# Optimization experiments

Measured on AMD Instinct MI355X. Metric: run time of the kernel, lower is better.

The kernel has to match this reference:

```python
import jax, jax.numpy as jnp
import numpy as np

N = 50000      # nodes
E = 1_600_000  # edges (avg degree 32)
G = 2000       # graphs in batch
H = 2          # attention heads
C = 64         # out_channels
IN = 64        # in_channels
NEG_SLOPE = 0.2


def setup_inputs() -> dict:
    key = jax.random.key(0)
    ks = jax.random.split(key, 6)
    x = jax.random.normal(ks[0], (N, IN), dtype=jnp.float32)
    edge_index = jax.random.randint(ks[1], (2, E), 0, N, dtype=jnp.int32)
    batch = jnp.sort(jax.random.randint(ks[2], (N,), 0, G, dtype=jnp.int32))
    # GATConv params: lin weight [H*C, IN] (glorot-ish), att vectors, bias [C]
    W = jax.random.normal(ks[3], (H * C, IN), dtype=jnp.float32) * (1.0 / np.sqrt(IN))
    att_src = jax.random.normal(ks[4], (1, H, C), dtype=jnp.float32) * 0.1
    att_dst = jax.random.normal(ks[5], (1, H, C), dtype=jnp.float32) * 0.1
    bias = jnp.zeros((C,), dtype=jnp.float32)
    return {"x": x, "edge_index": edge_index, "batch": batch,
            "W": W, "att_src": att_src, "att_dst": att_dst, "bias": bias}


def reference(x, edge_index, batch, W, att_src, att_dst, bias):
    # --- GATConv (PyG semantics: add_self_loops=True, concat=False -> head mean + bias) ---
    loops = jnp.arange(N, dtype=edge_index.dtype)
    src = jnp.concatenate([edge_index[0], loops])  # [E+N]
    dst = jnp.concatenate([edge_index[1], loops])  # [E+N]

    xp = (x @ W.T).reshape(N, H, C)                 # projected node feats [N,H,C]
    a_src = jnp.sum(xp * att_src, axis=-1)          # [N,H]
    a_dst = jnp.sum(xp * att_dst, axis=-1)          # [N,H]

    e = jax.nn.leaky_relu(a_src[src] + a_dst[dst], NEG_SLOPE)  # [E+N,H]
    # segment softmax over incoming edges of each destination node
    m = jax.ops.segment_max(e, dst, num_segments=N)            # [N,H]
    e = jnp.exp(e - m[dst])
    s = jax.ops.segment_sum(e, dst, num_segments=N)            # [N,H]
    alpha = e / s[dst]                                         # [E+N,H]

    msg = xp[src] * alpha[:, :, None]                          # [E+N,H,C]
    out = jax.ops.segment_sum(msg, dst, num_segments=N)        # [N,H,C]
    h_nodes = out.mean(axis=1) + bias                          # [N,C]

    # --- global_mean_pool ---
    sums = jax.ops.segment_sum(h_nodes, batch, num_segments=G)                     # [G,C]
    cnt = jax.ops.segment_sum(jnp.ones((N, 1), h_nodes.dtype), batch, num_segments=G)
    h_graphs = sums / jnp.maximum(cnt, 1.0)                                        # [G,C]
    return (h_nodes, h_graphs)
```

## Files before the change

### kernel.cpp

```cpp
#include <hip/hip_runtime.h>
#include <hip/hip_bf16.h>

#define H 2
#define C 64
#define IN_CH 64
#define HC (H*C)
#define NEG_SLOPE 0.2f
#define NBUCK_MAX 1024
#define SBLK 512
#define BKT 64
#define CAP 3072

__global__ __launch_bounds__(128) void proj_kernel(
    const float* __restrict__ x, const float* __restrict__ W,
    const float* __restrict__ att_src, const float* __restrict__ att_dst,
    const int* __restrict__ batch, __hip_bfloat16* __restrict__ xp,
    float* __restrict__ asrc, float* __restrict__ adst, int* __restrict__ cnt,
    int* __restrict__ gbeg, int N, int nbuck, int G) {
    int t = threadIdx.x;
    if (blockIdx.x == 0)
        for (int i = t; i < nbuck; i += 128) cnt[i] = 0;
    {
        int i = blockIdx.x * 128 + t;
        if (i < N) {
            int bi = batch[i];
            if (i == 0) {
                for (int g = 0; g <= bi; g++) gbeg[g] = 0;
            } else {
                int bp = batch[i - 1];
                for (int g = bp + 1; g <= bi; g++) gbeg[g] = i;
            }
            if (i == N - 1)
                for (int g = bi + 1; g <= G; g++) gbeg[g] = N;
        }
    }
    float w[64];
    const float4* wr = reinterpret_cast<const float4*>(W + (size_t)t * IN_CH);
#pragma unroll
    for (int q = 0; q < 16; q++) {
        float4 v = wr[q];
        w[4 * q] = v.x; w[4 * q + 1] = v.y; w[4 * q + 2] = v.z; w[4 * q + 3] = v.w;
    }
    float a_s = att_src[t], a_d = att_dst[t];
    int lane = t & 63, head = t >> 6;
    for (int n = blockIdx.x; n < N; n += gridDim.x) {
        const float* xr = x + (size_t)n * IN_CH;
        float acc = 0.f;
#pragma unroll
        for (int k = 0; k < 64; k++) acc = fmaf(w[k], xr[k], acc);
        xp[(size_t)n * HC + t] = __float2bfloat16(acc);
        float as = acc * a_s, ad = acc * a_d;
#pragma unroll
        for (int d = 32; d > 0; d >>= 1) {
            as += __shfl_xor(as, d, 64);
            ad += __shfl_xor(ad, d, 64);
        }
        if (lane == 0) {
            asrc[(size_t)n * H + head] = as;
            adst[(size_t)n * H + head] = ad;
        }
    }
}

__global__ __launch_bounds__(256) void scatter_kernel(
    const int* __restrict__ edge, int* __restrict__ cnt,
    int* __restrict__ staged, int N, int E) {
    const int tid = threadIdx.x, bid = blockIdx.x;
    const int nbuck = (N + BKT - 1) / BKT;
    const int chunkE = (E + SBLK - 1) / SBLK;
    const int* srcE = edge;
    const int* dstE = edge + E;
    __shared__ int lh[NBUCK_MAX], bse[NBUCK_MAX], lcur[NBUCK_MAX];
    for (int i = tid; i < nbuck; i += 256) { lh[i] = 0; lcur[i] = 0; }
    __syncthreads();
    int beg = bid * chunkE, end = min(beg + chunkE, E);
    for (int i = beg + tid; i < end; i += 256)
        atomicAdd(&lh[dstE[i] >> 6], 1);
    __syncthreads();
    for (int i = tid; i < nbuck; i += 256)
        bse[i] = atomicAdd(&cnt[i], lh[i]);
    __syncthreads();
    for (int i = beg + tid; i < end; i += 256) {
        int s = srcE[i], d = dstE[i];
        int b = d >> 6;
        int l = atomicAdd(&lcur[b], 1);
        staged[(size_t)b * CAP + bse[b] + l] = s | ((d & 63) << 20);
    }
}

template<int NB>
__device__ __forceinline__ void gfma(const char* __restrict__ xb,
                                     const int* __restrict__ si,
                                     const float* __restrict__ swl,
                                     uint laneoff, float& accx, float& accy) {
    uint bu[NB];
#pragma unroll
    for (int j = 0; j < NB; j++) {
        uint boff = (uint)si[j] + laneoff;
        bu[j] = *reinterpret_cast<const uint*>(xb + boff);
    }
#pragma unroll
    for (int j = 0; j < NB; j++) {
        float w = swl[2 * j];
        accx = fmaf(w, __uint_as_float(bu[j] << 16), accx);
        accy = fmaf(w, __uint_as_float(bu[j] & 0xffff0000u), accy);
    }
}

__global__ __launch_bounds__(256, 4) void csragg_kernel(
    const __hip_bfloat16* __restrict__ xp, const float* __restrict__ asrc,
    const float* __restrict__ adst, const int* __restrict__ cnt,
    const int* __restrict__ staged_all, const float* __restrict__ bias,
    float* __restrict__ out, int N) {
    __shared__ int lcsr[CAP];
    __shared__ int loff[BKT + 1];
    __shared__ int lh[BKT], cur[BKT];
    __shared__ int sidx[4][32];
    __shared__ float swf[4][64];
    int b = blockIdx.x, tid = threadIdx.x;
    int lane = tid & 63, wid = tid >> 6;
    int size = cnt[b];
    const int* st = staged_all + (size_t)b * CAP;
    if (tid < BKT) lh[tid] = 0;
    __syncthreads();
    for (int i = tid; i < size; i += 256)
        atomicAdd(&lh[st[i] >> 20], 1);
    __syncthreads();
    if (wid == 0) {
        int v = lh[lane];
        int inc = v;
#pragma unroll
        for (int d = 1; d < 64; d <<= 1) {
            int u = __shfl_up(inc, d, 64);
            if (lane >= d) inc += u;
        }
        loff[lane] = inc - v;
        cur[lane] = inc - v;
        if (lane == 63) loff[BKT] = inc;
    }
    __syncthreads();
    for (int i = tid; i < size; i += 256) {
        int e = st[i];
        int pos = atomicAdd(&cur[e >> 20], 1);
        lcsr[pos] = (e & 0xFFFFF) << 8;
    }
    __syncthreads();
    const uint* xpw = reinterpret_cast<const uint*>(xp);
    const char* xb = reinterpret_cast<const char*>(xp);
    int cl = lane & 31, hsel = lane >> 5;
    uint laneoff = (uint)lane * 4u;
    int* si = sidx[wid];
    float* swl = swf[wid] + hsel;
    for (int k = 0; k < 16; k++) {
        int nd = wid * 16 + k;
        int n = b * BKT + nd;
        if (n >= N) break;
        int o0 = loff[nd];
        int deg = loff[nd + 1] - o0;
        float adh = adst[2 * n + hsel];
        float es = asrc[2 * n + hsel] + adh;
        es = (es > 0.f) ? es : NEG_SLOPE * es;
        float wself = __expf(es);
        float ssum = (cl == 0) ? wself : 0.f;
        uint u = xpw[(size_t)n * 64 + lane];
        float accx = wself * __uint_as_float(u << 16);
        float accy = wself * __uint_as_float(u & 0xffff0000u);
        for (int base = 0; base < deg; base += 32) {
            int i = base + cl;
            int boff = 0;
            float w = 0.f;
            if (i < deg) {
                boff = lcsr[o0 + i];
                float t = asrc[(boff >> 7) + hsel] + adh;
                t = (t > 0.f) ? t : NEG_SLOPE * t;
                w = __expf(t);
            }
            ssum += w;
            if (!hsel) si[cl] = boff;
            swl[2 * cl] = w;
            int nb = min(deg - base, 32);
            if (nb > 16) gfma<32>(xb, si, swl, laneoff, accx, accy);
            else         gfma<16>(xb, si, swl, laneoff, accx, accy);
        }
#pragma unroll
        for (int d = 16; d > 0; d >>= 1) ssum += __shfl_xor(ssum, d, 64);
        float inv = 1.f / ssum;
        accx *= inv;
        accy *= inv;
        float ox = 0.5f * (accx + __shfl_xor(accx, 32, 64));
        float oy = 0.5f * (accy + __shfl_xor(accy, 32, 64));
        if (lane < 32) {
            float vx = ox + bias[2 * cl];
            float vy = oy + bias[2 * cl + 1];
            *reinterpret_cast<float2*>(out + (size_t)n * C + 2 * cl) =
                make_float2(vx, vy);
        }
    }
}

__global__ __launch_bounds__(256) void pool_kernel(const float* __restrict__ hn,
                                                   const int* __restrict__ gbeg,
                                                   float* __restrict__ outG, int G) {
    int g = blockIdx.x;
    int c = threadIdx.x & 63, r = threadIdx.x >> 6;
    int beg = gbeg[g], end = gbeg[g + 1];
    float s = 0.f;
    for (int n = beg + r; n < end; n += 4) s += hn[(size_t)n * C + c];
    __shared__ float red[256];
    red[threadIdx.x] = s;
    __syncthreads();
    if (r == 0) {
        float tot = red[c] + red[64 + c] + red[128 + c] + red[192 + c];
        outG[(size_t)g * C + c] = tot / fmaxf((float)(end - beg), 1.f);
    }
}

extern "C" void kernel_launch(void* const* d_in, const int* in_sizes, int n_in,
                              void* d_out, int out_size, void* d_ws, size_t ws_size,
                              hipStream_t stream) {
    const float* x       = (const float*)d_in[0];
    const int*   edge    = (const int*)d_in[1];
    const int*   batch   = (const int*)d_in[2];
    const float* W       = (const float*)d_in[3];
    const float* att_src = (const float*)d_in[4];
    const float* att_dst = (const float*)d_in[5];
    const float* bias    = (const float*)d_in[6];

    int N = in_sizes[0] / IN_CH;
    int E = in_sizes[1] / 2;
    int G = out_size / C - N;
    int nbuck = (N + BKT - 1) / BKT;

    char* p = (char*)d_ws;
    auto alloc = [&](size_t bytes) {
        char* r = p;
        p += (bytes + 255) & ~(size_t)255;
        return r;
    };
    __hip_bfloat16* xp = (__hip_bfloat16*)alloc((size_t)N * HC * 2);
    float* asrc    = (float*)alloc((size_t)N * H * 4);
    float* adst    = (float*)alloc((size_t)N * H * 4);
    int*   cnt     = (int*)alloc((size_t)nbuck * 4);
    int*   staged  = (int*)alloc((size_t)nbuck * CAP * 4);
    int*   gbeg    = (int*)alloc((size_t)(G + 1) * 4);

    proj_kernel<<<2048, 128, 0, stream>>>(x, W, att_src, att_dst, batch, xp, asrc, adst,
                                          cnt, gbeg, N, nbuck, G);
    scatter_kernel<<<SBLK, 256, 0, stream>>>(edge, cnt, staged, N, E);
    csragg_kernel<<<nbuck, 256, 0, stream>>>(xp, asrc, adst, cnt, staged, bias,
                                             (float*)d_out, N);
    pool_kernel<<<G, 256, 0, stream>>>((const float*)d_out, gbeg,
                                       (float*)d_out + (size_t)N * C, G);
}
```

Baseline: 203.8 us.

## Merge projection and edge-scatter kernels into one launch with block specialization

The projection and edge bucket-scatter kernels are combined into one launch. The first 512 blocks do the scatter (now with 128 threads each instead of 256) and the remaining 2048 blocks do the projection, so the two independent stages can run at the same time. The bucket-count zeroing moves from the projection kernel to a hipMemsetAsync, because the scatter blocks now need cnt already cleared. This saves one kernel boundary and lets the stages overlap, but the scatter blocks have half the threads and the memset adds a small operation to the stream.

```diff
diff --git a/kernel.cpp b/kernel.cpp
--- a/kernel.cpp
+++ b/kernel.cpp
@@ -8,20 +8,44 @@
 #define NEG_SLOPE 0.2f
 #define NBUCK_MAX 1024
 #define SBLK 512
+#define PBLK 2048
 #define BKT 64
 #define CAP 3072
 
-__global__ __launch_bounds__(128) void proj_kernel(
+__global__ __launch_bounds__(128) void fused_kernel(
     const float* __restrict__ x, const float* __restrict__ W,
     const float* __restrict__ att_src, const float* __restrict__ att_dst,
-    const int* __restrict__ batch, __hip_bfloat16* __restrict__ xp,
-    float* __restrict__ asrc, float* __restrict__ adst, int* __restrict__ cnt,
-    int* __restrict__ gbeg, int N, int nbuck, int G) {
-    int t = threadIdx.x;
-    if (blockIdx.x == 0)
-        for (int i = t; i < nbuck; i += 128) cnt[i] = 0;
+    const int* __restrict__ batch, const int* __restrict__ edge,
+    __hip_bfloat16* __restrict__ xp, float* __restrict__ asrc,
+    float* __restrict__ adst, int* __restrict__ cnt, int* __restrict__ staged,
+    int* __restrict__ gbeg, int N, int E, int G, int nbuck) {
+    const int t = threadIdx.x;
+    if (blockIdx.x < SBLK) {
+        const int bid = blockIdx.x;
+        const int chunkE = (E + SBLK - 1) / SBLK;
+        const int* srcE = edge;
+        const int* dstE = edge + E;
+        __shared__ int lh[NBUCK_MAX], bse[NBUCK_MAX], lcur[NBUCK_MAX];
+        for (int i = t; i < nbuck; i += 128) { lh[i] = 0; lcur[i] = 0; }
+        __syncthreads();
+        int beg = bid * chunkE, end = min(beg + chunkE, E);
+        for (int i = beg + t; i < end; i += 128)
+            atomicAdd(&lh[dstE[i] >> 6], 1);
+        __syncthreads();
+        for (int i = t; i < nbuck; i += 128)
+            bse[i] = atomicAdd(&cnt[i], lh[i]);
+        __syncthreads();
+        for (int i = beg + t; i < end; i += 128) {
+            int s = srcE[i], d = dstE[i];
+            int b = d >> 6;
+            int l = atomicAdd(&lcur[b], 1);
+            staged[(size_t)b * CAP + bse[b] + l] = s | ((d & 63) << 20);
+        }
+        return;
+    }
+    int pb = blockIdx.x - SBLK;
     {
-        int i = blockIdx.x * 128 + t;
+        int i = pb * 128 + t;
         if (i < N) {
             int bi = batch[i];
             if (i == 0) {
@@ -43,7 +67,7 @@
     }
     float a_s = att_src[t], a_d = att_dst[t];
     int lane = t & 63, head = t >> 6;
-    for (int n = blockIdx.x; n < N; n += gridDim.x) {
+    for (int n = pb; n < N; n += PBLK) {
         const float* xr = x + (size_t)n * IN_CH;
         float acc = 0.f;
 #pragma unroll
@@ -59,32 +83,6 @@
             asrc[(size_t)n * H + head] = as;
             adst[(size_t)n * H + head] = ad;
         }
-    }
-}
-
-__global__ __launch_bounds__(256) void scatter_kernel(
-    const int* __restrict__ edge, int* __restrict__ cnt,
-    int* __restrict__ staged, int N, int E) {
-    const int tid = threadIdx.x, bid = blockIdx.x;
-    const int nbuck = (N + BKT - 1) / BKT;
-    const int chunkE = (E + SBLK - 1) / SBLK;
-    const int* srcE = edge;
-    const int* dstE = edge + E;
-    __shared__ int lh[NBUCK_MAX], bse[NBUCK_MAX], lcur[NBUCK_MAX];
-    for (int i = tid; i < nbuck; i += 256) { lh[i] = 0; lcur[i] = 0; }
-    __syncthreads();
-    int beg = bid * chunkE, end = min(beg + chunkE, E);
-    for (int i = beg + tid; i < end; i += 256)
-        atomicAdd(&lh[dstE[i] >> 6], 1);
-    __syncthreads();
-    for (int i = tid; i < nbuck; i += 256)
-        bse[i] = atomicAdd(&cnt[i], lh[i]);
-    __syncthreads();
-    for (int i = beg + tid; i < end; i += 256) {
-        int s = srcE[i], d = dstE[i];
-        int b = d >> 6;
-        int l = atomicAdd(&lcur[b], 1);
-        staged[(size_t)b * CAP + bse[b] + l] = s | ((d & 63) << 20);
     }
 }
 
@@ -244,9 +242,10 @@
     int*   staged  = (int*)alloc((size_t)nbuck * CAP * 4);
     int*   gbeg    = (int*)alloc((size_t)(G + 1) * 4);
 
-    proj_kernel<<<2048, 128, 0, stream>>>(x, W, att_src, att_dst, batch, xp, asrc, adst,
-                                          cnt, gbeg, N, nbuck, G);
-    scatter_kernel<<<SBLK, 256, 0, stream>>>(edge, cnt, staged, N, E);
+    hipMemsetAsync(cnt, 0, (size_t)nbuck * 4, stream);
+    fused_kernel<<<SBLK + PBLK, 128, 0, stream>>>(x, W, att_src, att_dst, batch, edge,
+                                                  xp, asrc, adst, cnt, staged, gbeg,
+                                                  N, E, G, nbuck);
     csragg_kernel<<<nbuck, 256, 0, stream>>>(xp, asrc, adst, cnt, staged, bias,
                                              (float*)d_out, N);
     pool_kernel<<<G, 256, 0, stream>>>((const float*)d_out, gbeg,
```

New measurement: 190.1 us, median of 2. 6.7% less time.
